# Kernel optimization log

Hardware: AMD Instinct MI355X
Metric: run time of the kernel (lower is better)

## Reference

```python
import jax, jax.numpy as jnp
import numpy as np

B, IN, H = 16384, 512, 1024

def _linear_params(key, fan_in, fan_out):
    k1, k2 = jax.random.split(key)
    bound = 1.0 / np.sqrt(fan_in)
    W = jax.random.uniform(k1, (fan_out, fan_in), jnp.float32, -bound, bound)
    b = jax.random.uniform(k2, (fan_out,), jnp.float32, -bound, bound)
    return W, b

def setup_inputs() -> dict:
    key = jax.random.key(0)
    ks = jax.random.split(key, 10)
    x = jax.random.normal(ks[0], (B, IN), jnp.float32)
    h_prev = jax.random.normal(ks[1], (B, H), jnp.float32)
    c_prev = jax.random.normal(ks[2], (B, H), jnp.float32)
    W_i, b_i = _linear_params(ks[3], IN + H, H)
    W_f, b_f = _linear_params(ks[4], IN + H, H)
    W_o, b_o = _linear_params(ks[5], IN + H, H)
    W_g, b_g = _linear_params(ks[6], IN + H, H)
    W_a, b_a = _linear_params(ks[7], H, 1)
    W_ht, b_ht = _linear_params(ks[8], IN, H)
    W_hg, b_hg = _linear_params(ks[9], IN, H)
    return dict(x=x, h_prev=h_prev, c_prev=c_prev,
                W_i=W_i, b_i=b_i, W_f=W_f, b_f=b_f, W_o=W_o, b_o=b_o,
                W_g=W_g, b_g=b_g, W_a=W_a, b_a=b_a,
                W_ht=W_ht, b_ht=b_ht, W_hg=W_hg, b_hg=b_hg)

def reference(x, h_prev, c_prev, W_i, b_i, W_f, b_f, W_o, b_o, W_g, b_g,
              W_a, b_a, W_ht, b_ht, W_hg, b_hg):
    combined = jnp.concatenate([x, h_prev], axis=1)  # [B, IN+H]
    # fuse 4 gate GEMMs into one concatenated-weight GEMM
    W_gates = jnp.concatenate([W_i, W_f, W_o, W_g], axis=0)  # [4H, IN+H]
    b_gates = jnp.concatenate([b_i, b_f, b_o, b_g], axis=0)  # [4H]
    gates = combined @ W_gates.T + b_gates                   # [B, 4H]
    i, f, o, g = jnp.split(gates, 4, axis=1)
    i = jax.nn.sigmoid(i)
    f = jax.nn.sigmoid(f)
    o = jax.nn.sigmoid(o)
    g = jnp.tanh(g)
    c = f * c_prev + i * g
    h = o * jnp.tanh(c)
    # attention: softmax over the batch dim (dim=0), logits [B, 1]
    attn_logits = h @ W_a.T + b_a                 # [B, 1]
    attn = jax.nn.softmax(attn_logits, axis=0)    # [B, 1]
    h = h * attn
    # highway merge
    t = x @ W_ht.T + b_ht
    gate = jax.nn.sigmoid(x @ W_hg.T + b_hg)
    h = gate * t + (1.0 - gate) * h
    # dropout in eval mode: identity
    return (h, c)
```

## Files before the change

kernel.cpp:

```cpp
#include <hip/hip_runtime.h>
#include <stdint.h>

#define B_  16384
#define IN_ 512
#define H_  1024
#define KC_ 1536

typedef unsigned short u16;
typedef __attribute__((ext_vector_type(4))) float f32x4;
typedef __attribute__((ext_vector_type(8))) short s16x8;


__device__ __forceinline__ u16 f2bf(float f) {
  union { float f; uint32_t u; } un; un.f = f;
  uint32_t u = un.u;
  uint32_t r = (u + 0x7FFFu + ((u >> 16) & 1u)) >> 16;
  return (u16)r;
}

__device__ __forceinline__ float fast_sigmoid(float x) {
  return 1.f / (1.f + __expf(-x));
}
__device__ __forceinline__ float fast_tanh(float x) {
  return 1.f - 2.f / (1.f + __expf(2.f * x));
}

__device__ __forceinline__ void mfma_bf16(f32x4& d, s16x8 a, s16x8 b) {
  asm volatile("v_mfma_f32_16x16x32_bf16 %0, %1, %2, %0" : "+v"(d) : "v"(a), "v"(b));
}

__device__ __forceinline__ void async_copy16(void* lds, const void* g) {
  __builtin_amdgcn_global_load_lds(
      (const __attribute__((address_space(1))) void*)g,
      (__attribute__((address_space(3))) void*)lds, 16, 0, 0);
}

__global__ __launch_bounds__(256)
void k0_convert(const float* __restrict__ x, const float* __restrict__ hprev,
                const float* __restrict__ Wi, const float* __restrict__ Wf,
                const float* __restrict__ Wo, const float* __restrict__ Wg,
                const float* __restrict__ Wht, const float* __restrict__ Whg,
                u16* __restrict__ comb, u16* __restrict__ wcat,
                u16* __restrict__ wht2)
{
  const int NC_COMB = (B_ * KC_) / 4;
  const int NC_WCAT = (4 * H_ * KC_) / 4;
  const int NC_WHT  = (2 * H_ * IN_) / 4;
  const int TOTAL = NC_COMB + NC_WCAT + NC_WHT;
  const int stride = gridDim.x * blockDim.x;

  for (int idx = blockIdx.x * blockDim.x + threadIdx.x; idx < TOTAL; idx += stride) {
    const float* src;
    u16* dst;
    if (idx < NC_COMB) {
      int row = idx / 384, cq = idx % 384;
      src = (cq < 128) ? (x + (size_t)row * IN_ + cq * 4)
                       : (hprev + (size_t)row * H_ + (cq - 128) * 4);
      dst = comb + (size_t)idx * 4;
    } else if (idx < NC_COMB + NC_WCAT) {
      int j = idx - NC_COMB;
      int g = j / 393216;
      int rem = j % 393216;
      const float* W = (g == 0) ? Wi : (g == 1) ? Wf : (g == 2) ? Wo : Wg;
      src = W + (size_t)rem * 4;
      dst = wcat + (size_t)j * 4;
    } else {
      int j = idx - NC_COMB - NC_WCAT;
      int m = j / 131072;
      int rem = j % 131072;
      src = (m ? Whg : Wht) + (size_t)rem * 4;
      dst = wht2 + (size_t)j * 4;
    }
    float4 v = *(const float4*)src;
    uint32_t p0 = (uint32_t)f2bf(v.x) | ((uint32_t)f2bf(v.y) << 16);
    uint32_t p1 = (uint32_t)f2bf(v.z) | ((uint32_t)f2bf(v.w) << 16);
    *(uint2*)dst = make_uint2(p0, p1);
  }
}

__global__ __launch_bounds__(512, 2)
void k1_gates8ph(const u16* __restrict__ comb, const u16* __restrict__ wcat,
                 const float* __restrict__ bi, const float* __restrict__ bf_,
                 const float* __restrict__ bo, const float* __restrict__ bg,
                 const float* __restrict__ c_prev,
                 float* __restrict__ c_out, float* __restrict__ h_pre)
{
  __shared__ __attribute__((aligned(128))) char lds[131072];

  const int tid = threadIdx.x;
  const int w = tid >> 6, lane = tid & 63;
  const int lrow = lane & 15, lkg = lane >> 4;
  const int wm = w >> 2, wn = w & 3;

  int bid = blockIdx.y * gridDim.x + blockIdx.x;
  int swz = (bid & 7) * 128 + (bid >> 3);
  const int bx = swz & 15, by = swz >> 4;
  const int m0 = by * 256, n0h = bx * 64;

  const u16* pA[2][2]; const u16* pB[2][2];
  int ldsA[2][2], ldsB[2][2];
#pragma unroll
  for (int h = 0; h < 2; ++h)
#pragma unroll
    for (int t = 0; t < 2; ++t) {
      int i = w * 128 + t * 64 + lane;
      int rh = i >> 3, c = i & 7;
      int cs = c ^ (rh & 7);
      int rt = h * 128 + rh;
      pA[h][t] = comb + (size_t)(m0 + rt) * KC_ + cs * 8;
      int g = (rt >> 4) & 3, hc = n0h + ((rt >> 6) << 4) + (rt & 15);
      pB[h][t] = wcat + ((size_t)(g * H_ + hc)) * KC_ + cs * 8;
      ldsA[h][t] = h * 16384 + (w * 128 + t * 64) * 16;
      ldsB[h][t] = 32768 + h * 16384 + (w * 128 + t * 64) * 16;
    }

  int aoff[8], boff[4], kx[2];
#pragma unroll
  for (int mr = 0; mr < 8; ++mr) aoff[mr] = (wm * 128 + mr * 16 + lrow) * 128;
#pragma unroll
  for (int fc = 0; fc < 4; ++fc) boff[fc] = 32768 + (wn * 64 + fc * 16 + lrow) * 128;
  kx[0] = ((lkg) ^ (lrow & 7)) << 4;
  kx[1] = ((4 + lkg) ^ (lrow & 7)) << 4;

  f32x4 acc[8][4];
#pragma unroll
  for (int i = 0; i < 8; ++i)
#pragma unroll
    for (int j = 0; j < 4; ++j) acc[i][j] = (f32x4){0.f, 0.f, 0.f, 0.f};

  {
    char* b0 = lds;
    char* b1 = lds + 65536;
#pragma unroll
    for (int h = 0; h < 2; ++h)
#pragma unroll
      for (int t = 0; t < 2; ++t) async_copy16(b0 + ldsA[h][t], pA[h][t]);
#pragma unroll
    for (int h = 0; h < 2; ++h)
#pragma unroll
      for (int t = 0; t < 2; ++t) async_copy16(b0 + ldsB[h][t], pB[h][t]);
#pragma unroll
    for (int h = 0; h < 2; ++h)
#pragma unroll
      for (int t = 0; t < 2; ++t) async_copy16(b1 + ldsB[h][t], pB[h][t] + 64);
    asm volatile("s_waitcnt vmcnt(4)" ::: "memory");
    __builtin_amdgcn_sched_barrier(0);
    __builtin_amdgcn_s_barrier();
  }

  for (int S = 0; S < 24; ++S) {
    const int cur = S & 1;
    char* bufc = lds + cur * 65536;
    char* bufo = lds + (cur ^ 1) * 65536;
    s16x8 bfr[4][2];
#pragma unroll
    for (int q = 0; q < 4; ++q) {
      s16x8 afr[2][2];
#pragma unroll
      for (int j = 0; j < 2; ++j)
#pragma unroll
        for (int kk = 0; kk < 2; ++kk)
          afr[j][kk] = *(const s16x8*)(bufc + aoff[2 * q + j] + kx[kk]);
      if (q == 0) {
#pragma unroll
        for (int fc = 0; fc < 4; ++fc)
#pragma unroll
          for (int kk = 0; kk < 2; ++kk)
            bfr[fc][kk] = *(const s16x8*)(bufc + boff[fc] + kx[kk]);
      }
      if (q == 0 && S < 23) {
        async_copy16(bufo + ldsA[0][0], pA[0][0] + (S + 1) * 64);
        async_copy16(bufo + ldsA[0][1], pA[0][1] + (S + 1) * 64);
      }
      if (q == 1 && S < 23) {
        async_copy16(bufo + ldsA[1][0], pA[1][0] + (S + 1) * 64);
        async_copy16(bufo + ldsA[1][1], pA[1][1] + (S + 1) * 64);
      }
      if (q == 2 && S < 22) {
        async_copy16(bufc + ldsB[0][0], pB[0][0] + (S + 2) * 64);
        async_copy16(bufc + ldsB[0][1], pB[0][1] + (S + 2) * 64);
      }
      if (q == 3 && S < 22) {
        async_copy16(bufc + ldsB[1][0], pB[1][0] + (S + 2) * 64);
        async_copy16(bufc + ldsB[1][1], pB[1][1] + (S + 2) * 64);
      }
      asm volatile("" ::: "memory");
      __builtin_amdgcn_sched_barrier(0);
      __builtin_amdgcn_s_barrier();
      asm volatile("s_waitcnt lgkmcnt(0)" ::: "memory");
      __builtin_amdgcn_sched_barrier(0);
      __builtin_amdgcn_s_setprio(1);
#pragma unroll
      for (int kk = 0; kk < 2; ++kk)
#pragma unroll
        for (int fc = 0; fc < 4; ++fc)
#pragma unroll
          for (int j = 0; j < 2; ++j)
            mfma_bf16(acc[2 * q + j][fc], afr[j][kk], bfr[fc][kk]);
      __builtin_amdgcn_s_setprio(0);
      if (q == 3) {
        if (S < 22) asm volatile("s_waitcnt vmcnt(4)" ::: "memory");
        else        asm volatile("s_waitcnt vmcnt(0)" ::: "memory");
      }
      asm volatile("" ::: "memory");
      __builtin_amdgcn_sched_barrier(0);
      __builtin_amdgcn_s_barrier();
    }
  }

  const int hcol = n0h + wn * 16 + lrow;
  const float vbi = bi[hcol], vbf = bf_[hcol], vbo = bo[hcol], vbg = bg[hcol];
#pragma unroll
  for (int mr = 0; mr < 8; ++mr) {
    const int row0 = m0 + wm * 128 + mr * 16 + lkg * 4;
#pragma unroll
    for (int r4 = 0; r4 < 4; ++r4) {
      const size_t off = (size_t)(row0 + r4) * H_ + hcol;
      float iv = fast_sigmoid(acc[mr][0][r4] + vbi);
      float fv = fast_sigmoid(acc[mr][1][r4] + vbf);
      float ov = fast_sigmoid(acc[mr][2][r4] + vbo);
      float gv = fast_tanh(acc[mr][3][r4] + vbg);
      float c = fv * c_prev[off] + iv * gv;
      c_out[off] = c;
      h_pre[off] = ov * fast_tanh(c);
    }
  }
}

__global__ __launch_bounds__(256)
void k2_logits(const float* __restrict__ h_pre, const float* __restrict__ Wa,
               const float* __restrict__ ba, float* __restrict__ e,
               float* __restrict__ partial)
{
  __shared__ float wsum[4];
  const int w = threadIdx.x >> 6, lane = threadIdx.x & 63;
  const int r = blockIdx.x * 4 + w;
  const float4* hp = (const float4*)(h_pre + (size_t)r * H_);
  const float4* wa = (const float4*)Wa;
  float s = 0.f;
#pragma unroll
  for (int j = 0; j < 4; ++j) {
    float4 hv = hp[lane * 4 + j];
    float4 wv = wa[lane * 4 + j];
    s += hv.x * wv.x + hv.y * wv.y + hv.z * wv.z + hv.w * wv.w;
  }
#pragma unroll
  for (int off = 32; off; off >>= 1) s += __shfl_xor(s, off);
  float ev = __expf(s + ba[0]);
  if (lane == 0) { e[r] = ev; wsum[w] = ev; }
  __syncthreads();
  if (threadIdx.x == 0) partial[blockIdx.x] = wsum[0] + wsum[1] + wsum[2] + wsum[3];
}

__global__ __launch_bounds__(256)
void k2_reduce(const float* __restrict__ partial, float* __restrict__ sum_slot)
{
  __shared__ float ws4[4];
  float s = 0.f;
  for (int i = threadIdx.x; i < 4096; i += 256) s += partial[i];
#pragma unroll
  for (int off = 32; off; off >>= 1) s += __shfl_xor(s, off);
  if ((threadIdx.x & 63) == 0) ws4[threadIdx.x >> 6] = s;
  __syncthreads();
  if (threadIdx.x == 0) sum_slot[0] = ws4[0] + ws4[1] + ws4[2] + ws4[3];
}

__global__ __launch_bounds__(256, 2)
void k3_highway(const u16* __restrict__ comb, const u16* __restrict__ wht2,
                const float* __restrict__ bht, const float* __restrict__ bhg,
                const float* __restrict__ e, const float* __restrict__ sum_slot,
                float* __restrict__ h_out)
{
  __shared__ __attribute__((aligned(128))) char lds[32768];
  char* lds_a = lds;
  char* lds_b = lds + 16384;

  const int tid = threadIdx.x;
  const int w = tid >> 6, lane = tid & 63;
  const int lrow = lane & 15, lkg = lane >> 4;
  const int wm = w >> 1, wn = w & 1;
  const int m0 = blockIdx.y * 128;
  const int h0 = blockIdx.x * 64;

  const u16* agp[4]; const u16* bgp[4];
  char* alp[4]; char* blp[4];
#pragma unroll
  for (int t = 0; t < 4; ++t) {
    int j = w * 256 + t * 64 + lane;
    int r = j >> 3, q = j & 7;
    int qs = q ^ (r & 7);
    agp[t] = comb + (size_t)(m0 + r) * KC_ + qs * 8;
    alp[t] = lds_a + (w * 256 + t * 64) * 16;
    int mat = (r >> 4) & 1, n = ((r >> 5) << 4) + (r & 15);
    bgp[t] = wht2 + ((size_t)(mat * H_ + h0 + n)) * IN_ + qs * 8;
    blp[t] = lds_b + (w * 256 + t * 64) * 16;
  }

  f32x4 acc[4][4];
#pragma unroll
  for (int i = 0; i < 4; ++i)
#pragma unroll
    for (int j = 0; j < 4; ++j) acc[i][j] = (f32x4){0.f, 0.f, 0.f, 0.f};

  const int sw = (lrow & 7) << 4;
  int aoff[4], boff[4];
#pragma unroll
  for (int fm = 0; fm < 4; ++fm) aoff[fm] = (wm * 64 + fm * 16 + lrow) * 128;
#pragma unroll
  for (int fc = 0; fc < 4; ++fc) boff[fc] = (wn * 64 + fc * 16 + lrow) * 128;

  for (int kt = 0; kt < IN_ / 64; ++kt) {
#pragma unroll
    for (int t = 0; t < 4; ++t) {
      async_copy16(alp[t], agp[t] + kt * 64);
      async_copy16(blp[t], bgp[t] + kt * 64);
    }
    __syncthreads();
#pragma unroll
    for (int ks = 0; ks < 2; ++ks) {
      const int koff = (ks * 64 + lkg * 16) ^ sw;
      s16x8 a[4], b[4];
#pragma unroll
      for (int fm = 0; fm < 4; ++fm) a[fm] = *(const s16x8*)(lds_a + aoff[fm] + koff);
#pragma unroll
      for (int fc = 0; fc < 4; ++fc) b[fc] = *(const s16x8*)(lds_b + boff[fc] + koff);
#pragma unroll
      for (int fm = 0; fm < 4; ++fm)
#pragma unroll
        for (int fc = 0; fc < 4; ++fc) mfma_bf16(acc[fm][fc], a[fm], b[fc]);
    }
    __syncthreads();
  }

  const float invs = 1.f / sum_slot[0];
  const int hA = h0 + wn * 32 + lrow;
  const float vbht0 = bht[hA], vbht1 = bht[hA + 16];
  const float vbhg0 = bhg[hA], vbhg1 = bhg[hA + 16];
#pragma unroll
  for (int fm = 0; fm < 4; ++fm) {
    const int row0 = m0 + wm * 64 + fm * 16 + lkg * 4;
#pragma unroll
    for (int r4 = 0; r4 < 4; ++r4) {
      const int row = row0 + r4;
      const float escale = e[row] * invs;
#pragma unroll
      for (int hc = 0; hc < 2; ++hc) {
        const int h = hA + hc * 16;
        const size_t off = (size_t)row * H_ + h;
        float tv = acc[fm][2 * hc][r4] + (hc ? vbht1 : vbht0);
        float gv = fast_sigmoid(acc[fm][2 * hc + 1][r4] + (hc ? vbhg1 : vbhg0));
        float ha = h_out[off] * escale;
        h_out[off] = gv * tv + (1.f - gv) * ha;
      }
    }
  }
}

extern "C" void kernel_launch(void* const* d_in, const int* in_sizes, int n_in,
                              void* d_out, int out_size, void* d_ws, size_t ws_size,
                              hipStream_t stream) {
  const float* x      = (const float*)d_in[0];
  const float* h_prev = (const float*)d_in[1];
  const float* c_prev = (const float*)d_in[2];
  const float* Wi  = (const float*)d_in[3];
  const float* bi  = (const float*)d_in[4];
  const float* Wf  = (const float*)d_in[5];
  const float* bf_ = (const float*)d_in[6];
  const float* Wo  = (const float*)d_in[7];
  const float* bo  = (const float*)d_in[8];
  const float* Wg  = (const float*)d_in[9];
  const float* bg  = (const float*)d_in[10];
  const float* Wa  = (const float*)d_in[11];
  const float* ba  = (const float*)d_in[12];
  const float* Wht = (const float*)d_in[13];
  const float* bht = (const float*)d_in[14];
  const float* Whg = (const float*)d_in[15];
  const float* bhg = (const float*)d_in[16];

  char* ws = (char*)d_ws;
  float* sum_slot = (float*)(ws + 0);
  float* e        = (float*)(ws + 256);
  u16* comb = (u16*)(ws + 65792);
  u16* wcat = (u16*)(ws + 50397440);
  u16* wht2 = (u16*)(ws + 62980352);
  float* partial = (float*)(ws + 65077504);

  float* h_out = (float*)d_out;
  float* c_out = (float*)d_out + (size_t)B_ * H_;

  hipLaunchKernelGGL(k0_convert, dim3(2048), dim3(256), 0, stream,
                     x, h_prev, Wi, Wf, Wo, Wg, Wht, Whg, comb, wcat, wht2);
  hipLaunchKernelGGL(k1_gates8ph, dim3(16, 64), dim3(512), 0, stream,
                     comb, wcat, bi, bf_, bo, bg, c_prev, c_out, h_out);
  hipLaunchKernelGGL(k2_logits, dim3(B_ / 4), dim3(256), 0, stream,
                     h_out, Wa, ba, e, partial);
  hipLaunchKernelGGL(k2_reduce, dim3(1), dim3(256), 0, stream,
                     partial, sum_slot);
  hipLaunchKernelGGL(k3_highway, dim3(H_ / 64, B_ / 128), dim3(256), 0, stream,
                     comb, wht2, bht, bhg, e, sum_slot, h_out);
}
```

Before: 532.1 us.

## Restructure gate GEMM pipeline with unrolled two-stage phases and reordered A-row mapping

Rewrites the gate GEMM main loop as a fully unrolled pair of buffer phases with explicit macros, so the prefetch schedule interleaves A and B tile loads across both LDS buffers with deeper outstanding loads (vmcnt 6). It also remaps which A rows each wave's fragments cover, so a wave's first four fragments come from the first 128-row half of the tile and its last four from the second half. The epilogue indexing is updated to match. The goal is better overlap of global-to-LDS copies with MFMA work and fewer loop-carried branches. The cost is more complex synchronisation and a risk of LDS hazards if the wait counts are wrong.

```diff
diff --git a/kernel.cpp b/kernel.cpp
--- a/kernel.cpp
+++ b/kernel.cpp
@@ -114,13 +114,15 @@
       ldsB[h][t] = 32768 + h * 16384 + (w * 128 + t * 64) * 16;
     }
 
-  int aoff[8], boff[4], kx[2];
-#pragma unroll
-  for (int mr = 0; mr < 8; ++mr) aoff[mr] = (wm * 128 + mr * 16 + lrow) * 128;
-#pragma unroll
-  for (int fc = 0; fc < 4; ++fc) boff[fc] = 32768 + (wn * 64 + fc * 16 + lrow) * 128;
-  kx[0] = ((lkg) ^ (lrow & 7)) << 4;
-  kx[1] = ((4 + lkg) ^ (lrow & 7)) << 4;
+  int aoff[8], boff[4];
+#pragma unroll
+  for (int f = 0; f < 8; ++f)
+    aoff[f] = ((f >> 2) * 128 + wm * 64 + (f & 3) * 16 + lrow) * 128;
+#pragma unroll
+  for (int fc = 0; fc < 4; ++fc)
+    boff[fc] = 32768 + (wn * 64 + fc * 16 + lrow) * 128;
+  const int kx0 = ((lkg) ^ (lrow & 7)) << 4;
+  const int kx1 = ((4 + lkg) ^ (lrow & 7)) << 4;
 
   f32x4 acc[8][4];
 #pragma unroll
@@ -128,98 +130,88 @@
 #pragma unroll
     for (int j = 0; j < 4; ++j) acc[i][j] = (f32x4){0.f, 0.f, 0.f, 0.f};
 
-  {
-    char* b0 = lds;
-    char* b1 = lds + 65536;
-#pragma unroll
-    for (int h = 0; h < 2; ++h)
-#pragma unroll
-      for (int t = 0; t < 2; ++t) async_copy16(b0 + ldsA[h][t], pA[h][t]);
-#pragma unroll
-    for (int h = 0; h < 2; ++h)
-#pragma unroll
-      for (int t = 0; t < 2; ++t) async_copy16(b0 + ldsB[h][t], pB[h][t]);
-#pragma unroll
-    for (int h = 0; h < 2; ++h)
-#pragma unroll
-      for (int t = 0; t < 2; ++t) async_copy16(b1 + ldsB[h][t], pB[h][t] + 64);
-    asm volatile("s_waitcnt vmcnt(4)" ::: "memory");
-    __builtin_amdgcn_sched_barrier(0);
-    __builtin_amdgcn_s_barrier();
-  }
-
-  for (int S = 0; S < 24; ++S) {
-    const int cur = S & 1;
-    char* bufc = lds + cur * 65536;
-    char* bufo = lds + (cur ^ 1) * 65536;
-    s16x8 bfr[4][2];
-#pragma unroll
-    for (int q = 0; q < 4; ++q) {
-      s16x8 afr[2][2];
-#pragma unroll
-      for (int j = 0; j < 2; ++j)
-#pragma unroll
-        for (int kk = 0; kk < 2; ++kk)
-          afr[j][kk] = *(const s16x8*)(bufc + aoff[2 * q + j] + kx[kk]);
-      if (q == 0) {
-#pragma unroll
-        for (int fc = 0; fc < 4; ++fc)
-#pragma unroll
-          for (int kk = 0; kk < 2; ++kk)
-            bfr[fc][kk] = *(const s16x8*)(bufc + boff[fc] + kx[kk]);
-      }
-      if (q == 0 && S < 23) {
-        async_copy16(bufo + ldsA[0][0], pA[0][0] + (S + 1) * 64);
-        async_copy16(bufo + ldsA[0][1], pA[0][1] + (S + 1) * 64);
-      }
-      if (q == 1 && S < 23) {
-        async_copy16(bufo + ldsA[1][0], pA[1][0] + (S + 1) * 64);
-        async_copy16(bufo + ldsA[1][1], pA[1][1] + (S + 1) * 64);
-      }
-      if (q == 2 && S < 22) {
-        async_copy16(bufc + ldsB[0][0], pB[0][0] + (S + 2) * 64);
-        async_copy16(bufc + ldsB[0][1], pB[0][1] + (S + 2) * 64);
-      }
-      if (q == 3 && S < 22) {
-        async_copy16(bufc + ldsB[1][0], pB[1][0] + (S + 2) * 64);
-        async_copy16(bufc + ldsB[1][1], pB[1][1] + (S + 2) * 64);
-      }
-      asm volatile("" ::: "memory");
-      __builtin_amdgcn_sched_barrier(0);
-      __builtin_amdgcn_s_barrier();
-      asm volatile("s_waitcnt lgkmcnt(0)" ::: "memory");
-      __builtin_amdgcn_sched_barrier(0);
-      __builtin_amdgcn_s_setprio(1);
-#pragma unroll
-      for (int kk = 0; kk < 2; ++kk)
-#pragma unroll
-        for (int fc = 0; fc < 4; ++fc)
-#pragma unroll
-          for (int j = 0; j < 2; ++j)
-            mfma_bf16(acc[2 * q + j][fc], afr[j][kk], bfr[fc][kk]);
-      __builtin_amdgcn_s_setprio(0);
-      if (q == 3) {
-        if (S < 22) asm volatile("s_waitcnt vmcnt(4)" ::: "memory");
-        else        asm volatile("s_waitcnt vmcnt(0)" ::: "memory");
-      }
-      asm volatile("" ::: "memory");
-      __builtin_amdgcn_sched_barrier(0);
-      __builtin_amdgcn_s_barrier();
-    }
-  }
+  char* const buf0 = lds;
+  char* const buf1 = lds + 65536;
+
+#define SA(bufp, h, T) { async_copy16((bufp) + ldsA[h][0], pA[h][0] + (T) * 64); \
+                         async_copy16((bufp) + ldsA[h][1], pA[h][1] + (T) * 64); }
+#define SB(bufp, h, T) { async_copy16((bufp) + ldsB[h][0], pB[h][0] + (T) * 64); \
+                         async_copy16((bufp) + ldsB[h][1], pB[h][1] + (T) * 64); }
+
+  SB(buf0, 0, 0) SB(buf0, 1, 0) SA(buf0, 0, 0) SA(buf0, 1, 0)
+  SB(buf1, 0, 1) SB(buf1, 1, 1) SA(buf1, 0, 1)
+  asm volatile("s_waitcnt vmcnt(6)" ::: "memory");
+  __builtin_amdgcn_sched_barrier(0);
+  __builtin_amdgcn_s_barrier();
+
+  s16x8 bfr[4][2];
+
+#define PHASE(Q, bufc, STAGE, TAILWAIT)                                        \
+  {                                                                            \
+    s16x8 a0k0 = *(const s16x8*)((bufc) + aoff[2*(Q)]     + kx0);              \
+    s16x8 a1k0 = *(const s16x8*)((bufc) + aoff[2*(Q) + 1] + kx0);              \
+    s16x8 a0k1 = *(const s16x8*)((bufc) + aoff[2*(Q)]     + kx1);              \
+    s16x8 a1k1 = *(const s16x8*)((bufc) + aoff[2*(Q) + 1] + kx1);              \
+    if ((Q) == 0) {                                                            \
+      _Pragma("unroll")                                                        \
+      for (int fc = 0; fc < 4; ++fc) {                                         \
+        bfr[fc][0] = *(const s16x8*)((bufc) + boff[fc] + kx0);                 \
+        bfr[fc][1] = *(const s16x8*)((bufc) + boff[fc] + kx1);                 \
+      }                                                                        \
+    }                                                                          \
+    STAGE;                                                                     \
+    __builtin_amdgcn_sched_barrier(0);                                         \
+    __builtin_amdgcn_s_barrier();                                              \
+    asm volatile("s_waitcnt lgkmcnt(0)" ::: "memory");                         \
+    __builtin_amdgcn_sched_barrier(0);                                         \
+    __builtin_amdgcn_s_setprio(1);                                             \
+    _Pragma("unroll")                                                          \
+    for (int fc = 0; fc < 4; ++fc) {                                           \
+      mfma_bf16(acc[2*(Q)][fc],     a0k0, bfr[fc][0]);                         \
+      mfma_bf16(acc[2*(Q) + 1][fc], a1k0, bfr[fc][0]);                         \
+    }                                                                          \
+    _Pragma("unroll")                                                          \
+    for (int fc = 0; fc < 4; ++fc) {                                           \
+      mfma_bf16(acc[2*(Q)][fc],     a0k1, bfr[fc][1]);                         \
+      mfma_bf16(acc[2*(Q) + 1][fc], a1k1, bfr[fc][1]);                         \
+    }                                                                          \
+    __builtin_amdgcn_s_setprio(0);                                             \
+    TAILWAIT;                                                                  \
+    __builtin_amdgcn_sched_barrier(0);                                         \
+    __builtin_amdgcn_s_barrier();                                              \
+  }
+
+  for (int i = 0; i < 12; ++i) {
+    const int t2 = 2 * i + 2, t3 = 2 * i + 3;
+    const bool more = (i < 11);
+    PHASE(0, buf0, { SA(buf1, 1, 2 * i + 1) }, {})
+    PHASE(1, buf0, { if (more) SB(buf0, 0, t2) }, {})
+    PHASE(2, buf0, { if (more) SB(buf0, 1, t2) }, {})
+    PHASE(3, buf0, { if (more) SA(buf0, 0, t2) },
+          { if (more) asm volatile("s_waitcnt vmcnt(6)" ::: "memory");
+            else      asm volatile("s_waitcnt vmcnt(0)" ::: "memory"); })
+    PHASE(0, buf1, { if (more) SA(buf0, 1, t2) }, {})
+    PHASE(1, buf1, { if (more) SB(buf1, 0, t3) }, {})
+    PHASE(2, buf1, { if (more) SB(buf1, 1, t3) }, {})
+    PHASE(3, buf1, { if (more) SA(buf1, 0, t3) },
+          { asm volatile("s_waitcnt vmcnt(6)" ::: "memory"); })
+  }
+#undef PHASE
+#undef SA
+#undef SB
 
   const int hcol = n0h + wn * 16 + lrow;
   const float vbi = bi[hcol], vbf = bf_[hcol], vbo = bo[hcol], vbg = bg[hcol];
 #pragma unroll
-  for (int mr = 0; mr < 8; ++mr) {
-    const int row0 = m0 + wm * 128 + mr * 16 + lkg * 4;
+  for (int f = 0; f < 8; ++f) {
+    const int row0 = m0 + (f >> 2) * 128 + wm * 64 + (f & 3) * 16 + lkg * 4;
 #pragma unroll
     for (int r4 = 0; r4 < 4; ++r4) {
       const size_t off = (size_t)(row0 + r4) * H_ + hcol;
-      float iv = fast_sigmoid(acc[mr][0][r4] + vbi);
-      float fv = fast_sigmoid(acc[mr][1][r4] + vbf);
-      float ov = fast_sigmoid(acc[mr][2][r4] + vbo);
-      float gv = fast_tanh(acc[mr][3][r4] + vbg);
+      float iv = fast_sigmoid(acc[f][0][r4] + vbi);
+      float fv = fast_sigmoid(acc[f][1][r4] + vbf);
+      float ov = fast_sigmoid(acc[f][2][r4] + vbo);
+      float gv = fast_tanh(acc[f][3][r4] + vbg);
       float c = fv * c_prev[off] + iv * gv;
       c_out[off] = c;
       h_pre[off] = ov * fast_tanh(c);
```

Result: no change. 542.5 us (+2.0%).
